# Optimization experiments

Hardware: AMD Instinct MI355X
Metric: run time of the kernel (lower is better)

## Reference

```python
import jax, jax.numpy as jnp
import numpy as np


def setup_inputs() -> dict:
    key = jax.random.key(0)
    k1, k2, k3, k4, k5 = jax.random.split(key, 5)
    B, C, H, W = 16, 256, 32, 32
    G = 4
    gd = C // G
    x = jax.random.normal(k1, (B, C, H, W), dtype=jnp.float32)
    # grouped 1x1 convs == per-group [gd, gd] linear maps (torch weight (C, C//G, 1, 1))
    s = 1.0 / np.sqrt(gd)
    wq = jax.random.normal(k2, (G, gd, gd), dtype=jnp.float32) * s
    wk = jax.random.normal(k3, (G, gd, gd), dtype=jnp.float32) * s
    wv = jax.random.normal(k4, (G, gd, gd), dtype=jnp.float32) * s
    wo = jax.random.normal(k5, (C, C), dtype=jnp.float32) * (1.0 / np.sqrt(C))
    return {"x": x, "wq": wq, "wk": wk, "wv": wv, "wo": wo}


def reference(x, wq, wk, wv, wo):
    B, C, H, W = x.shape
    G, gd = wq.shape[0], wq.shape[1]
    N = H * W
    xg = x.reshape(B, G, gd, N)  # split channels into groups, flatten spatial
    # grouped 1x1 conv projections: out[d] = sum_c w[d,c] * x[c] per group
    Q = jnp.einsum('bgcn,gdc->bgdn', xg, wq)
    K = jnp.einsum('bgcn,gdc->bgdn', xg, wk)
    V = jnp.einsum('bgcn,gdc->bgdn', xg, wv)
    scale = 1.0 / (float(gd) ** 0.5)
    # scores: Q^T K over channel dim -> [B, G, N, N]
    scores = jnp.einsum('bgdn,bgdm->bgnm', Q, K) * scale
    attn = jax.nn.softmax(scores, axis=-1)
    # out[d, n] = sum_m attn[n, m] * V[d, m]  (== (attn @ V^T)^T in torch code)
    out = jnp.einsum('bgnm,bgdm->bgdn', attn, V)
    out = out.reshape(B, C, H, W)
    # out_proj: dense 1x1 conv over all channels
    return jnp.einsum('bchw,dc->bdhw', out, wo)
```

## Files before the change

kernel.cpp:

```cpp
#include <hip/hip_runtime.h>
#include <hip/hip_bf16.h>


typedef __bf16 bf16x8 __attribute__((ext_vector_type(8)));
typedef short s16x8 __attribute__((ext_vector_type(8)));
typedef float f32x4 __attribute__((ext_vector_type(4)));

__device__ __forceinline__ unsigned short f2b(float f) {
  unsigned int u = __builtin_bit_cast(unsigned int, f);
  u += 0x7fffu + ((u >> 16) & 1u);
  return (unsigned short)(u >> 16);
}
__device__ __forceinline__ unsigned short bf16u(float f) {
  return __builtin_bit_cast(unsigned short, __float2bfloat16(f));
}
__device__ __forceinline__ f32x4 mfma16(s16x8 a, s16x8 b, f32x4 c) {
  return __builtin_amdgcn_mfma_f32_16x16x32_bf16(
      __builtin_bit_cast(bf16x8, a), __builtin_bit_cast(bf16x8, b), c, 0, 0, 0);
}
__device__ __forceinline__ void gload16(const void* g, void* l) {
  __builtin_amdgcn_global_load_lds((const __attribute__((address_space(1))) void*)g,
                                   (__attribute__((address_space(3))) void*)l, 16, 0, 0);
}
__device__ __forceinline__ void stage8k(const unsigned short* g, short* l, int wid, int lane) {
  gload16(g + wid * 1024 + lane * 8,       l + wid * 1024);
  gload16(g + wid * 1024 + 512 + lane * 8, l + wid * 1024 + 512);
}

__global__ void prep_kernel(const float* __restrict__ wq, const float* __restrict__ wk,
                            const float* __restrict__ wv, const float* __restrict__ wo,
                            unsigned short* __restrict__ Mts, unsigned short* __restrict__ Ub) {
  int id = blockIdx.x * 256 + threadIdx.x;
  if (blockIdx.x < 64) {
    int g = id >> 12, e = (id >> 6) & 63, c = id & 63;
    const float* q = wq + g * 4096;
    const float* k = wk + g * 4096;
    float acc = 0.f;
    for (int d = 0; d < 64; ++d) acc += q[d * 64 + c] * k[d * 64 + e];
    Mts[g * 4096 + e * 64 + (c ^ ((e & 7) << 3))] = f2b(acc * 0.125f * 1.4426950408889634f);
  } else {
    int i = id - 16384;
    int o = i >> 8, gc = i & 255, g = gc >> 6, c = gc & 63;
    const float* v = wv + g * 4096;
    const float* w = wo + o * 256 + g * 64;
    float acc = 0.f;
    for (int d = 0; d < 64; ++d) acc += w[d] * v[d * 64 + c];
    Ub[i] = f2b(acc);
  }
}

__global__ __launch_bounds__(256) void cvt_kernel(const float* __restrict__ x,
                                                  unsigned short* __restrict__ XbT,
                                                  unsigned short* __restrict__ Xbs) {
  __shared__ __align__(16) short T[64][72];
  const int f = blockIdx.x;
  const int xcd = f & 7;
  const int idx = f >> 3;
  const int head = ((idx & 7) << 3) | xcd;
  const int tile = idx >> 3;
  const int chunk = head * 16 + tile;
  const int t0 = tile * 64;
  const int tid = threadIdx.x;
  const float* Xg = x + (size_t)head * 65536 + t0;
  for (int i = 0; i < 4; ++i) {
    int row = i * 16 + (tid >> 4);
    int col = (tid & 15) * 4;
    float4 v = *(const float4*)(Xg + (size_t)row * 1024 + col);
    ushort4 s4 = make_ushort4(f2b(v.x), f2b(v.y), f2b(v.z), f2b(v.w));
    *(ushort4*)&T[row][col] = s4;
  }
  __syncthreads();
  unsigned short* oT = XbT + (size_t)chunk * 4096;
  unsigned short* oC = Xbs + (size_t)chunk * 4096;
  for (int p = 0; p < 2; ++p) {
    int idx2 = p * 256 + tid;
    int rr = idx2 >> 3, j = idx2 & 7;
    int sb = (j ^ (rr & 7)) * 8;
    unsigned short w[8];
    for (int i = 0; i < 8; ++i) w[i] = (unsigned short)T[sb + i][rr];
    *(s16x8*)(oT + rr * 64 + j * 8) = *(s16x8*)w;
    s16x8 rv = *(const s16x8*)&T[rr][sb];
    *(s16x8*)(oC + rr * 64 + j * 8) = rv;
  }
}

__global__ __launch_bounds__(256, 2)
void attn_kernel(const unsigned short* __restrict__ XbT, const unsigned short* __restrict__ Xbs,
                 const unsigned short* __restrict__ Mts, unsigned short* __restrict__ Ast) {
  __shared__ __align__(16) short XtB[3][4096];
  __shared__ __align__(16) short XcB[3][4096];
  __shared__ __align__(16) short Pb[128 * 72];

  const int f = blockIdx.x;
  const int bg = (f & 7) + ((f >> 6) << 3);
  const int n0 = ((f >> 3) & 7) * 128;
  const int tid = threadIdx.x;
  const int wid = tid >> 6;
  const int lane = tid & 63;
  const int l15 = lane & 15, l4 = lane >> 4;
  const int swz = (l15 & 7) << 3;
  const unsigned short* xtg = XbT + (size_t)bg * 65536;
  const unsigned short* xcg = Xbs + (size_t)bg * 65536;
  short* Ps = Pb;

  stage8k(Mts + (bg & 3) * 4096, &XcB[0][0], wid, lane);
  stage8k(xtg + (size_t)(n0 >> 6) * 4096, &XtB[0][0], wid, lane);
  stage8k(xtg + (size_t)((n0 >> 6) + 1) * 4096, &XtB[1][0], wid, lane);
  __syncthreads();

  s16x8 qpB[2][2];
  {
    s16x8 bm[4][2];
    for (int eb = 0; eb < 4; ++eb)
      for (int kc = 0; kc < 2; ++kc)
        bm[eb][kc] = *(const s16x8*)&XcB[0][(eb * 16 + l15) * 64 + ((kc * 32 + l4 * 8) ^ swz)];
    for (int nt = 0; nt < 2; ++nt) {
      int q = wid * 32 + nt * 16;
      int h = q >> 6, rl = (q & 63) + l15;
      int rsw = ((rl & 7) << 3);
      s16x8 a0 = *(const s16x8*)&XtB[h][rl * 64 + ((l4 * 8) ^ rsw)];
      s16x8 a1 = *(const s16x8*)&XtB[h][rl * 64 + ((32 + l4 * 8) ^ rsw)];
      for (int eb = 0; eb < 4; ++eb) {
        f32x4 acc = {0.f, 0.f, 0.f, 0.f};
        acc = mfma16(a0, bm[eb][0], acc);
        acc = mfma16(a1, bm[eb][1], acc);
        for (int r = 0; r < 4; ++r)
          Ps[(q + 4 * l4 + r) * 72 + eb * 16 + l15] = (short)bf16u(acc[r]);
      }
    }
  }
  asm volatile("s_waitcnt lgkmcnt(0)" ::: "memory");
  __builtin_amdgcn_sched_barrier(0);
  for (int nt = 0; nt < 2; ++nt)
    for (int kc = 0; kc < 2; ++kc)
      qpB[nt][kc] = *(const s16x8*)&Ps[(wid * 32 + nt * 16 + l15) * 72 + kc * 32 + l4 * 8];
  __syncthreads();

  stage8k(xtg,        &XtB[0][0], wid, lane);
  stage8k(xcg,        &XcB[0][0], wid, lane);
  stage8k(xtg + 4096, &XtB[1][0], wid, lane);
  stage8k(xcg + 4096, &XcB[1][0], wid, lane);

  float rowSp[2] = {0.f, 0.f};
  f32x4 acc[2][4];
  for (int nt = 0; nt < 2; ++nt)
    for (int cb = 0; cb < 4; ++cb) acc[nt][cb] = (f32x4){0.f, 0.f, 0.f, 0.f};

#define STEP(K, VMC)                                                                    \
  {                                                                                     \
    asm volatile("s_waitcnt vmcnt(" VMC ")" ::: "memory");                              \
    __builtin_amdgcn_s_barrier();                                                       \
    __builtin_amdgcn_sched_barrier(0);                                                  \
    if ((K) < 14) {                                                                     \
      stage8k(xtg + (size_t)((K) + 2) * 4096, &XtB[((K) + 2) % 3][0], wid, lane);       \
      stage8k(xcg + (size_t)((K) + 2) * 4096, &XcB[((K) + 2) % 3][0], wid, lane);       \
    }                                                                                   \
    const int cs = (K) % 3;                                                             \
    s16x8 xt[4][2], ax[4][2];                                                           \
    for (int mb = 0; mb < 4; ++mb) {                                                    \
      int rm = mb * 16 + l15;                                                           \
      xt[mb][0] = *(const s16x8*)&XtB[cs][rm * 64 + ((l4 * 8) ^ swz)];                  \
      xt[mb][1] = *(const s16x8*)&XtB[cs][rm * 64 + ((32 + l4 * 8) ^ swz)];             \
      ax[mb][0] = *(const s16x8*)&XcB[cs][rm * 64 + ((l4 * 8) ^ swz)];                  \
      ax[mb][1] = *(const s16x8*)&XcB[cs][rm * 64 + ((32 + l4 * 8) ^ swz)];             \
    }                                                                                   \
    f32x4 s[2][4];                                                                      \
    for (int nt = 0; nt < 2; ++nt)                                                      \
      for (int mb = 0; mb < 4; ++mb) {                                                  \
        f32x4 a = {0.f, 0.f, 0.f, 0.f};                                                 \
        a = mfma16(xt[mb][0], qpB[nt][0], a);                                           \
        a = mfma16(xt[mb][1], qpB[nt][1], a);                                           \
        s[nt][mb] = a;                                                                  \
      }                                                                                 \
    for (int nt = 0; nt < 2; ++nt) {                                                    \
      const int prow = (wid * 32 + nt * 16 + l15) * 72;                                 \
      float ps = 0.f;                                                                   \
      for (int mb = 0; mb < 4; ++mb) {                                                  \
        float p0 = __builtin_amdgcn_exp2f(s[nt][mb][0]);                                \
        float p1 = __builtin_amdgcn_exp2f(s[nt][mb][1]);                                \
        float p2 = __builtin_amdgcn_exp2f(s[nt][mb][2]);                                \
        float p3 = __builtin_amdgcn_exp2f(s[nt][mb][3]);                                \
        ps += (p0 + p1) + (p2 + p3);                                                    \
        ushort4 pk = make_ushort4(bf16u(p0), bf16u(p1), bf16u(p2), bf16u(p3));          \
        *(ushort4*)&Ps[prow + mb * 16 + l4 * 4] = pk;                                   \
      }                                                                                 \
      rowSp[nt] += ps;                                                                  \
    }                                                                                   \
    asm volatile("s_waitcnt lgkmcnt(0)" ::: "memory");                                  \
    __builtin_amdgcn_sched_barrier(0);                                                  \
    for (int nt = 0; nt < 2; ++nt) {                                                    \
      const int prow = (wid * 32 + nt * 16 + l15) * 72;                                 \
      s16x8 pb0 = *(const s16x8*)&Ps[prow + l4 * 8];                                    \
      s16x8 pb1 = *(const s16x8*)&Ps[prow + 32 + l4 * 8];                               \
      for (int cb = 0; cb < 4; ++cb) {                                                  \
        acc[nt][cb] = mfma16(ax[cb][0], pb0, acc[nt][cb]);                              \
        acc[nt][cb] = mfma16(ax[cb][1], pb1, acc[nt][cb]);                              \
      }                                                                                 \
    }                                                                                   \
  }

  STEP(0, "4")  STEP(1, "4")  STEP(2, "4")  STEP(3, "4")
  STEP(4, "4")  STEP(5, "4")  STEP(6, "4")  STEP(7, "4")
  STEP(8, "4")  STEP(9, "4")  STEP(10, "4") STEP(11, "4")
  STEP(12, "4") STEP(13, "4") STEP(14, "4") STEP(15, "0")
#undef STEP

  const int b = bg >> 2, g = bg & 3;
  for (int nt = 0; nt < 2; ++nt) {
    float t = rowSp[nt];
    t += __shfl_xor(t, 16, 64);
    t += __shfl_xor(t, 32, 64);
    float inv = 1.f / t;
    int n = n0 + wid * 32 + nt * 16 + l15;
    unsigned short* Ag = Ast + ((size_t)(b * 1024 + n)) * 256 + g * 64;
    for (int cb = 0; cb < 4; ++cb) {
      f32x4 v = acc[nt][cb];
      ushort4 pk = make_ushort4(bf16u(v[0] * inv), bf16u(v[1] * inv),
                                bf16u(v[2] * inv), bf16u(v[3] * inv));
      *(ushort4*)(Ag + cb * 16 + l4 * 4) = pk;
    }
  }
}

__global__ __launch_bounds__(256, 2)
void proj_kernel(const unsigned short* __restrict__ Ub, const unsigned short* __restrict__ Ast,
                 float* __restrict__ out) {
  const int b = blockIdx.z;
  const int o0 = blockIdx.y * 128;
  const int n0 = blockIdx.x * 128;
  const int tid = threadIdx.x;
  const int wid = tid >> 6;
  const int lane = tid & 63;
  const int l15 = lane & 15, l4 = lane >> 4;
  const int ow = o0 + (wid & 1) * 64;
  const int nw = n0 + (wid >> 1) * 64;
  const unsigned short* A_ = Ast + ((size_t)b * 1024 + nw) * 256;

  f32x4 acc[4][4];
  for (int i = 0; i < 4; ++i)
    for (int j = 0; j < 4; ++j) acc[i][j] = (f32x4){0.f, 0.f, 0.f, 0.f};

  for (int kc = 0; kc < 8; ++kc) {
    s16x8 af[4], bfr[4];
    for (int ob = 0; ob < 4; ++ob)
      af[ob] = *(const s16x8*)(Ub + (size_t)(ow + ob * 16 + l15) * 256 + kc * 32 + l4 * 8);
    for (int nb = 0; nb < 4; ++nb)
      bfr[nb] = *(const s16x8*)(A_ + (size_t)(nb * 16 + l15) * 256 + kc * 32 + l4 * 8);
    for (int ob = 0; ob < 4; ++ob)
      for (int nb = 0; nb < 4; ++nb)
        acc[ob][nb] = mfma16(af[ob], bfr[nb], acc[ob][nb]);
  }
  float* O = out + ((size_t)b * 256 + ow) * 1024 + nw;
  for (int ob = 0; ob < 4; ++ob)
    for (int r = 0; r < 4; ++r)
      for (int nb = 0; nb < 4; ++nb)
        O[(size_t)(ob * 16 + l4 * 4 + r) * 1024 + nb * 16 + l15] = acc[ob][nb][r];
}

extern "C" void kernel_launch(void* const* d_in, const int* in_sizes, int n_in,
                              void* d_out, int out_size, void* d_ws, size_t ws_size,
                              hipStream_t stream) {
  const float* x  = (const float*)d_in[0];
  const float* wq = (const float*)d_in[1];
  const float* wk = (const float*)d_in[2];
  const float* wv = (const float*)d_in[3];
  const float* wo = (const float*)d_in[4];
  float* out = (float*)d_out;
  char* ws = (char*)d_ws;
  unsigned short* XbT = (unsigned short*)(ws);
  unsigned short* Xbs = (unsigned short*)(ws + 8388608);
  unsigned short* Mts = (unsigned short*)(ws + 16777216);
  unsigned short* Ub  = (unsigned short*)(ws + 16777216 + 32768);
  unsigned short* Ast = (unsigned short*)(ws + 16777216 + 163840);

  prep_kernel<<<320, 256, 0, stream>>>(wq, wk, wv, wo, Mts, Ub);
  cvt_kernel<<<1024, 256, 0, stream>>>(x, XbT, Xbs);
  attn_kernel<<<512, 256, 0, stream>>>(XbT, Xbs, Mts, Ast);
  proj_kernel<<<dim3(8, 2, 16), 256, 0, stream>>>(Ub, Ast, out);
}
```

Before: 55.70 us.

## Keep softmax probabilities in registers via K16 MFMA and merge prep/convert launches

```diff
diff --git a/kernel.cpp b/kernel.cpp
--- a/kernel.cpp
+++ b/kernel.cpp
@@ -4,6 +4,7 @@
 
 typedef __bf16 bf16x8 __attribute__((ext_vector_type(8)));
 typedef short s16x8 __attribute__((ext_vector_type(8)));
+typedef short s16x4 __attribute__((ext_vector_type(4)));
 typedef float f32x4 __attribute__((ext_vector_type(4)));
 
 __device__ __forceinline__ unsigned short f2b(float f) {
@@ -18,6 +19,9 @@
   return __builtin_amdgcn_mfma_f32_16x16x32_bf16(
       __builtin_bit_cast(bf16x8, a), __builtin_bit_cast(bf16x8, b), c, 0, 0, 0);
 }
+__device__ __forceinline__ f32x4 mfma16k16(s16x4 a, s16x4 b, f32x4 c) {
+  return __builtin_amdgcn_mfma_f32_16x16x16bf16_1k(a, b, c, 0, 0, 0);
+}
 __device__ __forceinline__ void gload16(const void* g, void* l) {
   __builtin_amdgcn_global_load_lds((const __attribute__((address_space(1))) void*)g,
                                    (__attribute__((address_space(3))) void*)l, 16, 0, 0);
@@ -27,41 +31,41 @@
   gload16(g + wid * 1024 + 512 + lane * 8, l + wid * 1024 + 512);
 }
 
-__global__ void prep_kernel(const float* __restrict__ wq, const float* __restrict__ wk,
-                            const float* __restrict__ wv, const float* __restrict__ wo,
-                            unsigned short* __restrict__ Mts, unsigned short* __restrict__ Ub) {
-  int id = blockIdx.x * 256 + threadIdx.x;
-  if (blockIdx.x < 64) {
-    int g = id >> 12, e = (id >> 6) & 63, c = id & 63;
-    const float* q = wq + g * 4096;
-    const float* k = wk + g * 4096;
-    float acc = 0.f;
-    for (int d = 0; d < 64; ++d) acc += q[d * 64 + c] * k[d * 64 + e];
-    Mts[g * 4096 + e * 64 + (c ^ ((e & 7) << 3))] = f2b(acc * 0.125f * 1.4426950408889634f);
-  } else {
-    int i = id - 16384;
-    int o = i >> 8, gc = i & 255, g = gc >> 6, c = gc & 63;
-    const float* v = wv + g * 4096;
-    const float* w = wo + o * 256 + g * 64;
-    float acc = 0.f;
-    for (int d = 0; d < 64; ++d) acc += w[d] * v[d * 64 + c];
-    Ub[i] = f2b(acc);
-  }
-}
-
-__global__ __launch_bounds__(256) void cvt_kernel(const float* __restrict__ x,
-                                                  unsigned short* __restrict__ XbT,
-                                                  unsigned short* __restrict__ Xbs) {
+__global__ __launch_bounds__(256) void cvt_prep_kernel(
+    const float* __restrict__ x, const float* __restrict__ wq, const float* __restrict__ wk,
+    const float* __restrict__ wv, const float* __restrict__ wo,
+    unsigned short* __restrict__ XbT, unsigned short* __restrict__ Xbs,
+    unsigned short* __restrict__ Mts, unsigned short* __restrict__ Ub) {
   __shared__ __align__(16) short T[64][72];
   const int f = blockIdx.x;
+  const int tid = threadIdx.x;
+  if (f >= 1024) {
+    int pb = f - 1024;
+    if (pb < 64) {
+      int id = pb * 256 + tid;
+      int g = id >> 12, e = (id >> 6) & 63, c = id & 63;
+      const float* q = wq + g * 4096;
+      const float* k = wk + g * 4096;
+      float acc = 0.f;
+      for (int d = 0; d < 64; ++d) acc += q[d * 64 + c] * k[d * 64 + e];
+      Mts[g * 4096 + e * 64 + (c ^ ((e & 7) << 3))] = f2b(acc * 0.125f * 1.4426950408889634f);
+    } else {
+      int i = (pb - 64) * 256 + tid;
+      int o = i >> 8, gc = i & 255, g = gc >> 6, c = gc & 63;
+      const float* v = wv + g * 4096;
+      const float* w = wo + o * 256 + g * 64;
+      float acc = 0.f;
+      for (int d = 0; d < 64; ++d) acc += w[d] * v[d * 64 + c];
+      Ub[i] = f2b(acc);
+    }
+    return;
+  }
   const int xcd = f & 7;
   const int idx = f >> 3;
   const int head = ((idx & 7) << 3) | xcd;
   const int tile = idx >> 3;
   const int chunk = head * 16 + tile;
-  const int t0 = tile * 64;
-  const int tid = threadIdx.x;
-  const float* Xg = x + (size_t)head * 65536 + t0;
+  const float* Xg = x + (size_t)head * 65536 + tile * 64;
   for (int i = 0; i < 4; ++i) {
     int row = i * 16 + (tid >> 4);
     int col = (tid & 15) * 4;
@@ -89,7 +93,6 @@
                  const unsigned short* __restrict__ Mts, unsigned short* __restrict__ Ast) {
   __shared__ __align__(16) short XtB[3][4096];
   __shared__ __align__(16) short XcB[3][4096];
-  __shared__ __align__(16) short Pb[128 * 72];
 
   const int f = blockIdx.x;
   const int bg = (f & 7) + ((f >> 6) << 3);
@@ -99,9 +102,9 @@
   const int lane = tid & 63;
   const int l15 = lane & 15, l4 = lane >> 4;
   const int swz = (l15 & 7) << 3;
+  const int l4h = l4 >> 1, l4l = (l4 & 1) * 4;
   const unsigned short* xtg = XbT + (size_t)bg * 65536;
   const unsigned short* xcg = Xbs + (size_t)bg * 65536;
-  short* Ps = Pb;
 
   stage8k(Mts + (bg & 3) * 4096, &XcB[0][0], wid, lane);
   stage8k(xtg + (size_t)(n0 >> 6) * 4096, &XtB[0][0], wid, lane);
@@ -120,20 +123,27 @@
       int rsw = ((rl & 7) << 3);
       s16x8 a0 = *(const s16x8*)&XtB[h][rl * 64 + ((l4 * 8) ^ rsw)];
       s16x8 a1 = *(const s16x8*)&XtB[h][rl * 64 + ((32 + l4 * 8) ^ rsw)];
+      short* Qs = (q >= 64) ? &XcB[2][0] : &XtB[2][0];
       for (int eb = 0; eb < 4; ++eb) {
         f32x4 acc = {0.f, 0.f, 0.f, 0.f};
         acc = mfma16(a0, bm[eb][0], acc);
         acc = mfma16(a1, bm[eb][1], acc);
-        for (int r = 0; r < 4; ++r)
-          Ps[(q + 4 * l4 + r) * 72 + eb * 16 + l15] = (short)bf16u(acc[r]);
+        for (int r = 0; r < 4; ++r) {
+          int qrow = q + 4 * l4 + r;
+          int cb2 = eb * 2 + (l15 >> 3);
+          Qs[(qrow & 63) * 64 + (((cb2 ^ (qrow & 7)) << 3) | (l15 & 7))] = (short)bf16u(acc[r]);
+        }
       }
     }
   }
   asm volatile("s_waitcnt lgkmcnt(0)" ::: "memory");
   __builtin_amdgcn_sched_barrier(0);
-  for (int nt = 0; nt < 2; ++nt)
+  for (int nt = 0; nt < 2; ++nt) {
+    int n = wid * 32 + nt * 16 + l15;
+    const short* Qs = (wid >= 2) ? &XcB[2][0] : &XtB[2][0];
     for (int kc = 0; kc < 2; ++kc)
-      qpB[nt][kc] = *(const s16x8*)&Ps[(wid * 32 + nt * 16 + l15) * 72 + kc * 32 + l4 * 8];
+      qpB[nt][kc] = *(const s16x8*)&Qs[(n & 63) * 64 + (((kc * 4 + l4) ^ (n & 7)) << 3)];
+  }
   __syncthreads();
 
   stage8k(xtg,        &XtB[0][0], wid, lane);
@@ -156,24 +166,27 @@
       stage8k(xcg + (size_t)((K) + 2) * 4096, &XcB[((K) + 2) % 3][0], wid, lane);       \
     }                                                                                   \
     const int cs = (K) % 3;                                                             \
-    s16x8 xt[4][2], ax[4][2];                                                           \
+    s16x8 xt0, xt1;                                                                     \
+    s16x4 ax4[4][4];                                                                    \
+    f32x4 s[2][4];                                                                      \
     for (int mb = 0; mb < 4; ++mb) {                                                    \
       int rm = mb * 16 + l15;                                                           \
-      xt[mb][0] = *(const s16x8*)&XtB[cs][rm * 64 + ((l4 * 8) ^ swz)];                  \
-      xt[mb][1] = *(const s16x8*)&XtB[cs][rm * 64 + ((32 + l4 * 8) ^ swz)];             \
-      ax[mb][0] = *(const s16x8*)&XcB[cs][rm * 64 + ((l4 * 8) ^ swz)];                  \
-      ax[mb][1] = *(const s16x8*)&XcB[cs][rm * 64 + ((32 + l4 * 8) ^ swz)];             \
-    }                                                                                   \
-    f32x4 s[2][4];                                                                      \
-    for (int nt = 0; nt < 2; ++nt)                                                      \
-      for (int mb = 0; mb < 4; ++mb) {                                                  \
+      xt0 = *(const s16x8*)&XtB[cs][rm * 64 + ((l4 * 8) ^ swz)];                        \
+      xt1 = *(const s16x8*)&XtB[cs][rm * 64 + ((32 + l4 * 8) ^ swz)];                   \
+      for (int nt = 0; nt < 2; ++nt) {                                                  \
         f32x4 a = {0.f, 0.f, 0.f, 0.f};                                                 \
-        a = mfma16(xt[mb][0], qpB[nt][0], a);                                           \
-        a = mfma16(xt[mb][1], qpB[nt][1], a);                                           \
+        a = mfma16(xt0, qpB[nt][0], a);                                                 \
+        a = mfma16(xt1, qpB[nt][1], a);                                                 \
         s[nt][mb] = a;                                                                  \
       }                                                                                 \
+    }                                                                                   \
+    for (int cb = 0; cb < 4; ++cb) {                                                    \
+      int rc = cb * 16 + l15;                                                           \
+      for (int mb = 0; mb < 4; ++mb)                                                    \
+        ax4[cb][mb] = *(const s16x4*)&XcB[cs][rc * 64 +                                 \
+                        (((mb * 2 + l4h) ^ (rc & 7)) << 3) + l4l];                      \
+    }                                                                                   \
     for (int nt = 0; nt < 2; ++nt) {                                                    \
-      const int prow = (wid * 32 + nt * 16 + l15) * 72;                                 \
       float ps = 0.f;                                                                   \
       for (int mb = 0; mb < 4; ++mb) {                                                  \
         float p0 = __builtin_amdgcn_exp2f(s[nt][mb][0]);                                \
@@ -181,21 +194,14 @@
         float p2 = __builtin_amdgcn_exp2f(s[nt][mb][2]);                                \
         float p3 = __builtin_amdgcn_exp2f(s[nt][mb][3]);                                \
         ps += (p0 + p1) + (p2 + p3);                                                    \
-        ushort4 pk = make_ushort4(bf16u(p0), bf16u(p1), bf16u(p2), bf16u(p3));          \
-        *(ushort4*)&Ps[prow + mb * 16 + l4 * 4] = pk;                                   \
+        unsigned int lo = (unsigned int)bf16u(p0) | ((unsigned int)bf16u(p1) << 16);    \
+        unsigned int hi = (unsigned int)bf16u(p2) | ((unsigned int)bf16u(p3) << 16);    \
+        uint2 pu; pu.x = lo; pu.y = hi;                                                 \
+        s16x4 pb = __builtin_bit_cast(s16x4, pu);                                       \
+        for (int cb = 0; cb < 4; ++cb)                                                  \
+          acc[nt][cb] = mfma16k16(ax4[cb][mb], pb, acc[nt][cb]);                        \
       }                                                                                 \
       rowSp[nt] += ps;                                                                  \
-    }                                                                                   \
-    asm volatile("s_waitcnt lgkmcnt(0)" ::: "memory");                                  \
-    __builtin_amdgcn_sched_barrier(0);                                                  \
-    for (int nt = 0; nt < 2; ++nt) {                                                    \
-      const int prow = (wid * 32 + nt * 16 + l15) * 72;                                 \
-      s16x8 pb0 = *(const s16x8*)&Ps[prow + l4 * 8];                                    \
-      s16x8 pb1 = *(const s16x8*)&Ps[prow + 32 + l4 * 8];                               \
-      for (int cb = 0; cb < 4; ++cb) {                                                  \
-        acc[nt][cb] = mfma16(ax[cb][0], pb0, acc[nt][cb]);                              \
-        acc[nt][cb] = mfma16(ax[cb][1], pb1, acc[nt][cb]);                              \
-      }                                                                                 \
     }                                                                                   \
   }
 
@@ -273,8 +279,7 @@
   unsigned short* Ub  = (unsigned short*)(ws + 16777216 + 32768);
   unsigned short* Ast = (unsigned short*)(ws + 16777216 + 163840);
 
-  prep_kernel<<<320, 256, 0, stream>>>(wq, wk, wv, wo, Mts, Ub);
-  cvt_kernel<<<1024, 256, 0, stream>>>(x, XbT, Xbs);
+  cvt_prep_kernel<<<1344, 256, 0, stream>>>(x, wq, wk, wv, wo, XbT, Xbs, Mts, Ub);
   attn_kernel<<<512, 256, 0, stream>>>(XbT, Xbs, Mts, Ast);
   proj_kernel<<<dim3(8, 2, 16), 256, 0, stream>>>(Ub, Ast, out);
 }
```

New measurement: 53.15 us. -4.6%, faster.
